# Performance work log

Measured on AMD Instinct MI355X. Metric: run time of the kernel, lower is better.

## Reference

```python
import jax, jax.numpy as jnp
import numpy as np

V, E, H, B, S, K, L = 32000, 512, 1024, 16, 128, 15, 1


def setup_inputs() -> dict:
    key = jax.random.key(0)
    ks = jax.random.split(key, 12)
    s = 0.02
    W_emb = jax.random.normal(ks[0], (V, E), jnp.float32) * s
    W_emb = W_emb.at[0].set(0.0)  # padding_idx=0
    return {
        "input_ids": jax.random.randint(ks[1], (B, S), 0, V),
        "hidden": jnp.zeros((L, B, H), jnp.float32),
        "stop_indicators": jax.random.randint(ks[2], (B, S), 0, 2),
        "W_emb": W_emb,
        "W_ih": jax.random.normal(ks[3], (H, E), jnp.float32) * s,
        "b_ih": jax.random.normal(ks[4], (H,), jnp.float32) * s,
        "W_hh": jax.random.normal(ks[5], (H, H), jnp.float32) * s,
        "b_hh": jax.random.normal(ks[6], (H,), jnp.float32) * s,
        "W_dec": jax.random.normal(ks[7], (V, H), jnp.float32) * s,
        "b_dec": jax.random.normal(ks[8], (V,), jnp.float32) * s,
        "beta": jax.random.uniform(ks[9], (K, V), jnp.float32),
        "theta": jax.random.uniform(ks[10], (K,), jnp.float32),
    }


def reference(input_ids, hidden, stop_indicators, W_emb, W_ih, b_ih, W_hh, b_hh,
              W_dec, b_dec, beta, theta):
    # Embedding lookup: [B, S, E]
    emb = W_emb[input_ids]
    xs = jnp.swapaxes(emb, 0, 1)  # [S, B, E] time-major for scan
    h0 = hidden[0]                # [B, H]

    # Elman RNN (tanh), single layer, batch_first semantics
    def step(h, x):
        h_new = jnp.tanh(x @ W_ih.T + b_ih + h @ W_hh.T + b_hh)
        return h_new, h_new

    hT, outs = jax.lax.scan(step, h0, xs)      # outs: [S, B, H]
    output = jnp.swapaxes(outs, 0, 1)          # [B, S, H]

    decoded = output @ W_dec.T + b_dec         # [B, S, V]

    # Topic additions: single fused GEMV theta @ beta (replaces per-vocab loop)
    topic_additions = theta @ beta             # [V]
    stop_mask = (stop_indicators == 0).astype(decoded.dtype)[..., None]  # [B,S,1]
    decoded = decoded + topic_additions * stop_mask

    return decoded, hT[None]  # hidden back as [layers=1, B, H]
```

## Files before the change

### kernel.cpp

```cpp
#include <hip/hip_runtime.h>
#include <stdint.h>

#define V_ 32000
#define E_ 512
#define H_ 1024
#define B_ 16
#define S_ 128
#define K_ 15

typedef float floatx4 __attribute__((ext_vector_type(4)));
typedef short shortx8 __attribute__((ext_vector_type(8)));
typedef __bf16 bf16x8 __attribute__((ext_vector_type(8)));

static __device__ __forceinline__ unsigned short f2b(float f) {
  union { float f; uint32_t u; } v; v.f = f;
  uint32_t u = v.u;
  u += 0x7FFFu + ((u >> 16) & 1u);
  return (unsigned short)(u >> 16);
}

static __device__ __forceinline__ shortx8 cvt8(floatx4 a, floatx4 b) {
  shortx8 r;
  r[0] = (short)f2b(a[0]); r[1] = (short)f2b(a[1]);
  r[2] = (short)f2b(a[2]); r[3] = (short)f2b(a[3]);
  r[4] = (short)f2b(b[0]); r[5] = (short)f2b(b[1]);
  r[6] = (short)f2b(b[2]); r[7] = (short)f2b(b[3]);
  return r;
}

static __device__ __forceinline__ floatx4 mfma_bf16(shortx8 a, shortx8 b, floatx4 c) {
  return __builtin_amdgcn_mfma_f32_16x16x32_bf16(
      __builtin_bit_cast(bf16x8, a), __builtin_bit_cast(bf16x8, b), c, 0, 0, 0);
}


__global__ void k_zero(int* __restrict__ p, int n) {
  int i = blockIdx.x * blockDim.x + threadIdx.x;
  if (i < n) p[i] = 0;
}

__global__ void k_topic(const float* __restrict__ beta, const float* __restrict__ theta,
                        float* __restrict__ topic) {
  int n = blockIdx.x * blockDim.x + threadIdx.x;
  float s = 0.f;
#pragma unroll
  for (int k = 0; k < K_; ++k) s += theta[k] * beta[k * V_ + n];
  topic[n] = s;
}

__global__ void k_cvt(const float* __restrict__ src, unsigned short* __restrict__ dst) {
  size_t i = (size_t)(blockIdx.x * blockDim.x + threadIdx.x) * 8;
  floatx4 f0 = *(const floatx4*)(src + i);
  floatx4 f1 = *(const floatx4*)(src + i + 4);
  *(shortx8*)(dst + i) = cvt8(f0, f1);
}

__global__ __launch_bounds__(256, 2) void k_gemm_pre(
    const int* __restrict__ ids, const float* __restrict__ W_emb,
    const float* __restrict__ W_ih, const float* __restrict__ b_ih,
    const float* __restrict__ b_hh, float* __restrict__ pre) {
  __shared__ unsigned short As[128 * 72];
  __shared__ unsigned short Bs[128 * 72];
  const int tid = threadIdx.x;
  const int gn0 = blockIdx.x * 128;
  const int gm0 = blockIdx.y * 128;
  const int wave = tid >> 6, lane = tid & 63;
  const int wm = (wave >> 1) * 64, wn = (wave & 1) * 64;
  const int lr = lane & 15, lg = lane >> 4;

  floatx4 acc[4][4];
#pragma unroll
  for (int i = 0; i < 4; ++i)
#pragma unroll
    for (int j = 0; j < 4; ++j) acc[i][j] = (floatx4)0.0f;

  for (int k0 = 0; k0 < E_; k0 += 64) {
#pragma unroll
    for (int c = 0; c < 4; ++c) {
      int q = c * 256 + tid;
      int row = q >> 3, kc = (q & 7) * 8;
      int m = gm0 + row;
      int id = ids[(m & 15) * S_ + (m >> 4)];
      const float* ga = W_emb + (size_t)id * E_ + k0 + kc;
      floatx4 a0 = *(const floatx4*)ga;
      floatx4 a1 = *(const floatx4*)(ga + 4);
      *(shortx8*)&As[row * 72 + kc] = cvt8(a0, a1);
      const float* gb = W_ih + (size_t)(gn0 + row) * E_ + k0 + kc;
      floatx4 c0 = *(const floatx4*)gb;
      floatx4 c1 = *(const floatx4*)(gb + 4);
      *(shortx8*)&Bs[row * 72 + kc] = cvt8(c0, c1);
    }
    __syncthreads();
#pragma unroll
    for (int ks = 0; ks < 64; ks += 32) {
      shortx8 af[4], bfr[4];
#pragma unroll
      for (int i = 0; i < 4; ++i)
        af[i] = *(const shortx8*)&As[(wm + i * 16 + lr) * 72 + ks + lg * 8];
#pragma unroll
      for (int j = 0; j < 4; ++j)
        bfr[j] = *(const shortx8*)&Bs[(wn + j * 16 + lr) * 72 + ks + lg * 8];
#pragma unroll
      for (int i = 0; i < 4; ++i)
#pragma unroll
        for (int j = 0; j < 4; ++j) acc[i][j] = mfma_bf16(af[i], bfr[j], acc[i][j]);
    }
    __syncthreads();
  }
#pragma unroll
  for (int i = 0; i < 4; ++i) {
#pragma unroll
    for (int r = 0; r < 4; ++r) {
      int m = gm0 + wm + i * 16 + lg * 4 + r;
#pragma unroll
      for (int j = 0; j < 4; ++j) {
        int n = gn0 + wn + j * 16 + lr;
        pre[(size_t)m * H_ + n] = acc[i][j][r] + b_ih[n] + b_hh[n];
      }
    }
  }
}

static __device__ __forceinline__ void gridbar(int* bar, int i) {
  __syncthreads();
  if (threadIdx.x == 0) {
    __threadfence();
    __hip_atomic_fetch_add(&bar[i], 1, __ATOMIC_ACQ_REL, __HIP_MEMORY_SCOPE_AGENT);
    while (__hip_atomic_load(&bar[i], __ATOMIC_ACQUIRE, __HIP_MEMORY_SCOPE_AGENT) < 64) {
      __builtin_amdgcn_s_sleep(1);
    }
  }
  __syncthreads();
}

__global__ __launch_bounds__(256, 1) void k_rnn(
    const float* __restrict__ hidden0, const float* __restrict__ W_hh,
    const float* __restrict__ pre, unsigned short* __restrict__ hb,
    unsigned short* __restrict__ act,
    float* __restrict__ hT_out,
    int* __restrict__ bar) {
  __shared__ unsigned short Bw[2048 * 8];
  __shared__ float red[4 * 64 * 4];
  const int tid = threadIdx.x, bid = blockIdx.x;
  const int wave = tid >> 6, lane = tid & 63;
  const int lr = lane & 15, lg = lane >> 4;

  for (int q = tid; q < 2048; q += 256) {
    int kstep = q >> 6, slot = q & 63;
    int n = bid * 16 + (slot & 15);
    int kb = kstep * 32 + (slot >> 4) * 8;
    const float* g = W_hh + (size_t)n * H_ + kb;
    floatx4 f0 = *(const floatx4*)g;
    floatx4 f1 = *(const floatx4*)(g + 4);
    *(shortx8*)&Bw[q * 8] = cvt8(f0, f1);
  }
  {
    int b = tid >> 4, n = bid * 16 + (tid & 15);
    hb[b * H_ + n] = f2b(hidden0[b * H_ + n]);
  }
  __threadfence();
  gridbar(bar, 0);

  for (int t = 0; t < S_; ++t) {
    const unsigned short* hcur = hb + (t & 1) * (B_ * H_);
    unsigned short* hnxt = hb + ((t + 1) & 1) * (B_ * H_);
    floatx4 acc = (floatx4)0.0f;
#pragma unroll
    for (int s = 0; s < 8; ++s) {
      int kstep = wave * 8 + s;
      int k = kstep * 32 + lg * 8;
      shortx8 af = *(const shortx8*)&hcur[lr * H_ + k];
      shortx8 bfr = *(const shortx8*)&Bw[(kstep * 64 + lane) * 8];
      acc = mfma_bf16(af, bfr, acc);
    }
    *(floatx4*)&red[(wave * 64 + lane) * 4] = acc;
    __syncthreads();
    {
      int l = tid & 63, r = tid >> 6;
      float s = red[(0 * 64 + l) * 4 + r] + red[(1 * 64 + l) * 4 + r] +
                red[(2 * 64 + l) * 4 + r] + red[(3 * 64 + l) * 4 + r];
      int b = ((l >> 4) * 4) + r;
      int n = bid * 16 + (l & 15);
      s += pre[((size_t)t * B_ + b) * H_ + n];
      float h = tanhf(s);
      unsigned short h16 = f2b(h);
      hnxt[b * H_ + n] = h16;
      act[((size_t)b * S_ + t) * H_ + n] = h16;
      if (t == S_ - 1) hT_out[b * H_ + n] = h;
    }
    gridbar(bar, t + 1);
  }
}

__global__ __launch_bounds__(256, 2) void k_gemm_dec(
    const unsigned short* __restrict__ A, const unsigned short* __restrict__ Bw,
    const float* __restrict__ b_dec, const float* __restrict__ topic,
    const int* __restrict__ stop, float* __restrict__ out) {
  __shared__ unsigned short As[128 * 72];
  __shared__ unsigned short Bs[128 * 72];
  const int tid = threadIdx.x;
  const int gn0 = blockIdx.x * 128;
  const int gm0 = blockIdx.y * 128;
  const int wave = tid >> 6, lane = tid & 63;
  const int wm = (wave >> 1) * 64, wn = (wave & 1) * 64;
  const int lr = lane & 15, lg = lane >> 4;

  floatx4 acc[4][4];
#pragma unroll
  for (int i = 0; i < 4; ++i)
#pragma unroll
    for (int j = 0; j < 4; ++j) acc[i][j] = (floatx4)0.0f;

  for (int k0 = 0; k0 < H_; k0 += 64) {
#pragma unroll
    for (int c = 0; c < 4; ++c) {
      int q = c * 256 + tid;
      int row = q >> 3, kc = (q & 7) * 8;
      *(shortx8*)&As[row * 72 + kc] =
          *(const shortx8*)(A + (size_t)(gm0 + row) * H_ + k0 + kc);
      *(shortx8*)&Bs[row * 72 + kc] =
          *(const shortx8*)(Bw + (size_t)(gn0 + row) * H_ + k0 + kc);
    }
    __syncthreads();
#pragma unroll
    for (int ks = 0; ks < 64; ks += 32) {
      shortx8 af[4], bfr[4];
#pragma unroll
      for (int i = 0; i < 4; ++i)
        af[i] = *(const shortx8*)&As[(wm + i * 16 + lr) * 72 + ks + lg * 8];
#pragma unroll
      for (int j = 0; j < 4; ++j)
        bfr[j] = *(const shortx8*)&Bs[(wn + j * 16 + lr) * 72 + ks + lg * 8];
#pragma unroll
      for (int i = 0; i < 4; ++i)
#pragma unroll
        for (int j = 0; j < 4; ++j) acc[i][j] = mfma_bf16(af[i], bfr[j], acc[i][j]);
    }
    __syncthreads();
  }
#pragma unroll
  for (int i = 0; i < 4; ++i) {
#pragma unroll
    for (int r = 0; r < 4; ++r) {
      int m = gm0 + wm + i * 16 + lg * 4 + r;
      float msk = (stop[m] == 0) ? 1.f : 0.f;
      size_t base = (size_t)m * V_;
#pragma unroll
      for (int j = 0; j < 4; ++j) {
        int n = gn0 + wn + j * 16 + lr;
        out[base + n] = acc[i][j][r] + b_dec[n] + topic[n] * msk;
      }
    }
  }
}

extern "C" void kernel_launch(void* const* d_in, const int* in_sizes, int n_in,
                              void* d_out, int out_size, void* d_ws, size_t ws_size,
                              hipStream_t stream) {
  (void)in_sizes; (void)n_in; (void)out_size; (void)ws_size;
  const int*   ids    = (const int*)d_in[0];
  const float* hidden = (const float*)d_in[1];
  const int*   stop   = (const int*)d_in[2];
  const float* W_emb  = (const float*)d_in[3];
  const float* W_ih   = (const float*)d_in[4];
  const float* b_ih   = (const float*)d_in[5];
  const float* W_hh   = (const float*)d_in[6];
  const float* b_hh   = (const float*)d_in[7];
  const float* W_dec  = (const float*)d_in[8];
  const float* b_dec  = (const float*)d_in[9];
  const float* beta   = (const float*)d_in[10];
  const float* theta  = (const float*)d_in[11];
  float* out = (float*)d_out;

  char* ws = (char*)d_ws;
  size_t off = 0;
  auto alloc = [&](size_t bytes) -> void* {
    void* p = ws + off;
    off = (off + bytes + 255) & ~(size_t)255;
    return p;
  };
  int* bar = (int*)alloc(512 * sizeof(int));
  float* topic = (float*)alloc((size_t)V_ * 4);
  float* pre = (float*)alloc((size_t)B_ * S_ * H_ * 4);
  unsigned short* act = (unsigned short*)alloc((size_t)B_ * S_ * H_ * 2);
  unsigned short* hb = (unsigned short*)alloc((size_t)2 * B_ * H_ * 2);
  unsigned short* wdec16 = (unsigned short*)alloc((size_t)V_ * H_ * 2);

  k_zero<<<dim3(1), dim3(512), 0, stream>>>(bar, 512);
  k_topic<<<dim3(V_ / 256), dim3(256), 0, stream>>>(beta, theta, topic);
  k_cvt<<<dim3((V_ * H_) / (256 * 8)), dim3(256), 0, stream>>>(W_dec, wdec16);
  k_gemm_pre<<<dim3(H_ / 128, (B_ * S_) / 128), dim3(256), 0, stream>>>(
      ids, W_emb, W_ih, b_ih, b_hh, pre);
  k_rnn<<<dim3(64), dim3(256), 0, stream>>>(hidden, W_hh, pre, hb, act,
                                            out + (size_t)B_ * S_ * V_, bar);
  k_gemm_dec<<<dim3(V_ / 128, (B_ * S_) / 128), dim3(256), 0, stream>>>(
      act, wdec16, b_dec, topic, stop, out);
}
```

Measured before the change: 1.314 ms.

## Restructure RNN recurrence: 16 blocks, register-resident W_hh, MFMA-ready hidden layout

The recurrent kernel now runs on 16 blocks instead of 64. Each wave owns 16 output columns across the full K=1024 and keeps its W_hh slice in registers as bf16, so the LDS cross-wave reduction and one __syncthreads per step go away. The hidden state is stored in a swizzled fragment-ready layout so each lane loads contiguous MFMA operands, and four independent accumulators break the MFMA dependency chain. Barrier counters are padded to separate cache lines and the final barrier is skipped. Fewer blocks should make each grid barrier cheaper, at the cost of less parallelism per step and much higher register pressure (32 shortx8 per lane).

```diff
diff --git a/kernel.cpp b/kernel.cpp
--- a/kernel.cpp
+++ b/kernel.cpp
@@ -121,74 +121,92 @@
   }
 }
 
-static __device__ __forceinline__ void gridbar(int* bar, int i) {
-  __syncthreads();
-  if (threadIdx.x == 0) {
-    __threadfence();
-    __hip_atomic_fetch_add(&bar[i], 1, __ATOMIC_ACQ_REL, __HIP_MEMORY_SCOPE_AGENT);
-    while (__hip_atomic_load(&bar[i], __ATOMIC_ACQUIRE, __HIP_MEMORY_SCOPE_AGENT) < 64) {
-      __builtin_amdgcn_s_sleep(1);
-    }
-  }
-  __syncthreads();
-}
-
 __global__ __launch_bounds__(256, 1) void k_rnn(
     const float* __restrict__ hidden0, const float* __restrict__ W_hh,
     const float* __restrict__ pre, unsigned short* __restrict__ hb,
     unsigned short* __restrict__ act,
     float* __restrict__ hT_out,
     int* __restrict__ bar) {
-  __shared__ unsigned short Bw[2048 * 8];
-  __shared__ float red[4 * 64 * 4];
   const int tid = threadIdx.x, bid = blockIdx.x;
-  const int wave = tid >> 6, lane = tid & 63;
+  const int lane = tid & 63, wave = tid >> 6;
   const int lr = lane & 15, lg = lane >> 4;
-
-  for (int q = tid; q < 2048; q += 256) {
-    int kstep = q >> 6, slot = q & 63;
-    int n = bid * 16 + (slot & 15);
-    int kb = kstep * 32 + (slot >> 4) * 8;
-    const float* g = W_hh + (size_t)n * H_ + kb;
+  const int nn = bid * 64 + wave * 16 + lr;
+
+  shortx8 bfr[32];
+#pragma unroll
+  for (int s = 0; s < 32; ++s) {
+    const float* g = W_hh + (size_t)nn * H_ + s * 32 + lg * 8;
     floatx4 f0 = *(const floatx4*)g;
     floatx4 f1 = *(const floatx4*)(g + 4);
-    *(shortx8*)&Bw[q * 8] = cvt8(f0, f1);
-  }
+    bfr[s] = cvt8(f0, f1);
+  }
+
   {
-    int b = tid >> 4, n = bid * 16 + (tid & 15);
-    hb[b * H_ + n] = f2b(hidden0[b * H_ + n]);
-  }
-  __threadfence();
-  gridbar(bar, 0);
+    int gt = (bid * 256 + tid) * 4;
+#pragma unroll
+    for (int u = 0; u < 4; ++u) {
+      int e = gt + u;
+      int b = e >> 10, n = e & 1023;
+      hb[(((n >> 5) * 64 + ((n >> 3) & 3) * 16 + b) << 3) + (n & 7)] = f2b(hidden0[e]);
+    }
+  }
+
+  __syncthreads();
+  if (tid == 0) {
+    __threadfence();
+    __hip_atomic_fetch_add(&bar[0], 1, __ATOMIC_ACQ_REL, __HIP_MEMORY_SCOPE_AGENT);
+    while (__hip_atomic_load(&bar[0], __ATOMIC_ACQUIRE, __HIP_MEMORY_SCOPE_AGENT) < 16)
+      __builtin_amdgcn_s_sleep(1);
+  }
+  __syncthreads();
+
+  const int sft = (((nn >> 5) * 64 + ((nn >> 3) & 3) * 16) << 3) + (nn & 7);
 
   for (int t = 0; t < S_; ++t) {
     const unsigned short* hcur = hb + (t & 1) * (B_ * H_);
     unsigned short* hnxt = hb + ((t + 1) & 1) * (B_ * H_);
-    floatx4 acc = (floatx4)0.0f;
-#pragma unroll
-    for (int s = 0; s < 8; ++s) {
-      int kstep = wave * 8 + s;
-      int k = kstep * 32 + lg * 8;
-      shortx8 af = *(const shortx8*)&hcur[lr * H_ + k];
-      shortx8 bfr = *(const shortx8*)&Bw[(kstep * 64 + lane) * 8];
-      acc = mfma_bf16(af, bfr, acc);
-    }
-    *(floatx4*)&red[(wave * 64 + lane) * 4] = acc;
-    __syncthreads();
-    {
-      int l = tid & 63, r = tid >> 6;
-      float s = red[(0 * 64 + l) * 4 + r] + red[(1 * 64 + l) * 4 + r] +
-                red[(2 * 64 + l) * 4 + r] + red[(3 * 64 + l) * 4 + r];
-      int b = ((l >> 4) * 4) + r;
-      int n = bid * 16 + (l & 15);
-      s += pre[((size_t)t * B_ + b) * H_ + n];
-      float h = tanhf(s);
+
+    float prer[4];
+#pragma unroll
+    for (int r = 0; r < 4; ++r)
+      prer[r] = pre[((size_t)t * B_ + lg * 4 + r) * H_ + nn];
+
+    floatx4 a0 = (floatx4)0.f, a1 = (floatx4)0.f, a2 = (floatx4)0.f, a3 = (floatx4)0.f;
+#pragma unroll
+    for (int s = 0; s < 32; s += 4) {
+      shortx8 f0 = *(const shortx8*)&hcur[((s + 0) * 64 + lane) * 8];
+      shortx8 f1 = *(const shortx8*)&hcur[((s + 1) * 64 + lane) * 8];
+      shortx8 f2 = *(const shortx8*)&hcur[((s + 2) * 64 + lane) * 8];
+      shortx8 f3 = *(const shortx8*)&hcur[((s + 3) * 64 + lane) * 8];
+      a0 = mfma_bf16(f0, bfr[s + 0], a0);
+      a1 = mfma_bf16(f1, bfr[s + 1], a1);
+      a2 = mfma_bf16(f2, bfr[s + 2], a2);
+      a3 = mfma_bf16(f3, bfr[s + 3], a3);
+    }
+    floatx4 acc = (a0 + a1) + (a2 + a3);
+
+#pragma unroll
+    for (int r = 0; r < 4; ++r) {
+      int b = lg * 4 + r;
+      float h = tanhf(acc[r] + prer[r]);
       unsigned short h16 = f2b(h);
-      hnxt[b * H_ + n] = h16;
-      act[((size_t)b * S_ + t) * H_ + n] = h16;
-      if (t == S_ - 1) hT_out[b * H_ + n] = h;
-    }
-    gridbar(bar, t + 1);
+      hnxt[sft + b * 8] = h16;
+      act[((size_t)b * S_ + t) * H_ + nn] = h16;
+      if (t == S_ - 1) hT_out[b * H_ + nn] = h;
+    }
+
+    if (t < S_ - 1) {
+      __syncthreads();
+      if (tid == 0) {
+        __threadfence();
+        __hip_atomic_fetch_add(&bar[(t + 1) * 32], 1, __ATOMIC_ACQ_REL,
+                               __HIP_MEMORY_SCOPE_AGENT);
+        while (__hip_atomic_load(&bar[(t + 1) * 32], __ATOMIC_ACQUIRE,
+                                 __HIP_MEMORY_SCOPE_AGENT) < 16)
+          __builtin_amdgcn_s_sleep(1);
+      }
+      __syncthreads();
+    }
   }
 }
 
@@ -279,19 +297,19 @@
     off = (off + bytes + 255) & ~(size_t)255;
     return p;
   };
-  int* bar = (int*)alloc(512 * sizeof(int));
+  int* bar = (int*)alloc(16384 * sizeof(int));
   float* topic = (float*)alloc((size_t)V_ * 4);
   float* pre = (float*)alloc((size_t)B_ * S_ * H_ * 4);
   unsigned short* act = (unsigned short*)alloc((size_t)B_ * S_ * H_ * 2);
   unsigned short* hb = (unsigned short*)alloc((size_t)2 * B_ * H_ * 2);
   unsigned short* wdec16 = (unsigned short*)alloc((size_t)V_ * H_ * 2);
 
-  k_zero<<<dim3(1), dim3(512), 0, stream>>>(bar, 512);
+  k_zero<<<dim3(32), dim3(512), 0, stream>>>(bar, 16384);
   k_topic<<<dim3(V_ / 256), dim3(256), 0, stream>>>(beta, theta, topic);
   k_cvt<<<dim3((V_ * H_) / (256 * 8)), dim3(256), 0, stream>>>(W_dec, wdec16);
   k_gemm_pre<<<dim3(H_ / 128, (B_ * S_) / 128), dim3(256), 0, stream>>>(
       ids, W_emb, W_ih, b_ih, b_hh, pre);
-  k_rnn<<<dim3(64), dim3(256), 0, stream>>>(hidden, W_hh, pre, hb, act,
+  k_rnn<<<dim3(16), dim3(256), 0, stream>>>(hidden, W_hh, pre, hb, act,
                                             out + (size_t)B_ * S_ * V_, bar);
   k_gemm_dec<<<dim3(V_ / 128, (B_ * S_) / 128), dim3(256), 0, stream>>>(
       act, wdec16, b_dec, topic, stop, out);
```

Measured after the change: 1.243 ms. 5.4% less time.
